# Optimization experiments

Measured on AMD Instinct MI355X. Metric: run time of the kernel, lower is better.

Reference implementation:

```python
import jax, jax.numpy as jnp
import numpy as np

K_SIZE = 7   # min_kernel_size (Parameter init value, clamped)
DIL = 2      # min_dilation (Parameter init value, clamped)


def conv2d(x, w, b):
    # x: (B, Cin, H, W), w: (Cout, Cin, kh, kw), stride 1, pad 1
    y = jax.lax.conv_general_dilated(
        x, w, window_strides=(1, 1), padding=((1, 1), (1, 1)),
        dimension_numbers=("NCHW", "OIHW", "NCHW"))
    return y + b[None, :, None, None]


def sincos_1d(length, dim, dtype):
    # standard sinusoidal encoding: (length, dim)
    half = dim // 2
    inv_freq = 1.0 / (10000.0 ** (jnp.arange(half, dtype=dtype) * 2.0 / dim))
    ang = jnp.arange(length, dtype=dtype)[:, None] * inv_freq[None, :]
    return jnp.concatenate([jnp.sin(ang), jnp.cos(ang)], axis=-1)


def positional_encoding_2d(H, W, C, dtype):
    # first C//2 channels encode height, last C//2 encode width -> (H, W, C)
    pe_h = sincos_1d(H, C // 2, dtype)  # (H, C/2)
    pe_w = sincos_1d(W, C // 2, dtype)  # (W, C/2)
    pe = jnp.concatenate([
        jnp.broadcast_to(pe_h[:, None, :], (H, W, C // 2)),
        jnp.broadcast_to(pe_w[None, :, :], (H, W, C // 2)),
    ], axis=-1)
    return pe


def na_indices(L, K, D):
    # NATTEN-style dilated neighborhood indices with border clamping.
    # Each position i attends within its dilation group g = i % D.
    i = jnp.arange(L)
    g = i % D
    r = i // D                       # rank within group
    Lg = (L - g + D - 1) // D        # group length
    start = jnp.clip(r - K // 2, 0, Lg - K)
    return g[:, None] + (start[:, None] + jnp.arange(K)[None, :]) * D  # (L, K)


def neighborhood_attention_2d(q, k, v, K, D):
    # q, k: (B, H, W, Cqk); v: (B, H, W, Cv); single head, scale = Cqk**-0.5
    B, H, W, Cqk = q.shape
    scale = jnp.asarray(Cqk, q.dtype) ** -0.5
    idx_h = na_indices(H, K, D)  # (H, K)
    idx_w = na_indices(W, K, D)  # (W, K)
    # gather neighborhood keys/values: (B, H, K, W, K, C)
    kn = k[:, idx_h][:, :, :, idx_w]
    vn = v[:, idx_h][:, :, :, idx_w]
    logits = jnp.einsum('bhwc,bhiwjc->bhwij', q * scale, kn)  # (B,H,W,K,K)
    p = jax.nn.softmax(logits.reshape(B, H, W, K * K), axis=-1)
    p = p.reshape(B, H, W, K, K)
    return jnp.einsum('bhwij,bhiwjc->bhwc', p, vn)


def setup_inputs() -> dict:
    key = jax.random.key(0)
    ks = jax.random.split(key, 4)
    B, Cin, H, W = 2, 64, 96, 96
    Ci, Co = 64, 128
    fan = Cin * 9
    s = (1.0 / fan) ** 0.5
    return {
        "x": jax.random.normal(ks[0], (B, Cin, H, W), dtype=jnp.float32),
        "wq": jax.random.normal(ks[1], (Ci, Cin, 3, 3), dtype=jnp.float32) * s,
        "bq": jnp.zeros((Ci,), dtype=jnp.float32),
        "wk": jax.random.normal(ks[2], (Ci, Cin, 3, 3), dtype=jnp.float32) * s,
        "bk": jnp.zeros((Ci,), dtype=jnp.float32),
        "wv": jax.random.normal(ks[3], (Co, Cin, 3, 3), dtype=jnp.float32) * s,
        "bv": jnp.zeros((Co,), dtype=jnp.float32),
    }


def reference(x, wq, bq, wk, bk, wv, bv):
    # Conv QKV (NCHW), then move to channels-last for attention
    q = jnp.transpose(conv2d(x, wq, bq), (0, 2, 3, 1))  # (B,H,W,Ci)
    k = jnp.transpose(conv2d(x, wk, bk), (0, 2, 3, 1))
    v = jnp.transpose(conv2d(x, wv, bv), (0, 2, 3, 1))  # (B,H,W,Co)
    B, H, W, Ci = q.shape
    pe = positional_encoding_2d(H, W, Ci, q.dtype)       # (H,W,Ci)
    pe_b = jnp.broadcast_to(pe[None], (B, H, W, Ci))
    q = jnp.concatenate([q, pe_b], axis=-1)              # (B,H,W,2*Ci)
    k = jnp.concatenate([k, pe_b], axis=-1)
    return neighborhood_attention_2d(q, k, v, K_SIZE, DIL)
```

## Files before the change

### kernel.cpp

```cpp
#include <hip/hip_runtime.h>
#include <math.h>

#define HWDIM 96
#define NPIX (HWDIM*HWDIM)
#define BATCH 2
#define CIN 64
#define CCAT 128

typedef __attribute__((ext_vector_type(8))) short bf16x8;
typedef __attribute__((ext_vector_type(4))) float f32x4;

__device__ __forceinline__ unsigned short f2bf(float f) {
    unsigned u = __builtin_bit_cast(unsigned, f);
    unsigned r = (u + 0x7FFFu + ((u >> 16) & 1u)) >> 16;
    return (unsigned short)r;
}

__global__ __launch_bounds__(256) void wb_kernel(
        const float* __restrict__ wq, const float* __restrict__ wk,
        const float* __restrict__ wv, unsigned short* __restrict__ wbT) {
    int base = blockIdx.x * 4096;
    int tid  = threadIdx.x;
    #pragma unroll
    for (int e = 0; e < 16; ++e) {
        int idx = base + e * 256 + tid;
        int t   = idx / (256 * 64);
        int rem = idx % (256 * 64);
        int co  = rem / 64;
        int ci  = rem % 64;
        float val;
        if (co < 64)        val = wq[(co * 64 + ci) * 9 + t];
        else if (co < 128)  val = wk[((co - 64) * 64 + ci) * 9 + t];
        else                val = wv[((co - 128) * 64 + ci) * 9 + t];
        wbT[(t * 256 + co) * 64 + ci] = f2bf(val);
    }
}

__global__ __launch_bounds__(256, 2) void conv_mfma(
        const float* __restrict__ x,
        const unsigned short* __restrict__ wbT,
        const float* __restrict__ bq, const float* __restrict__ bk,
        const float* __restrict__ bv,
        unsigned short* __restrict__ Qb, unsigned short* __restrict__ Kb,
        unsigned short* __restrict__ Vb) {
    __shared__ unsigned short xs[3 * 50 * 72];
    int bx      = blockIdx.x;
    int spatial = (bx & 7) * 48 + (bx >> 3);
    int b    = spatial / 192;
    int hh   = spatial % 192;
    int h    = hh >> 1;
    int w0   = (hh & 1) * 48;
    int co0  = blockIdx.y * 128;
    int tid  = threadIdx.x;

    #pragma unroll
    for (int g = 0; g < 5; ++g) {
        float vv[8];
        int   dst[8];
        bool  ok[8];
        #pragma unroll
        for (int e = 0; e < 8; ++e) {
            int i  = tid + (g * 8 + e) * 256;
            ok[e]  = (i < 9600);
            int ii = ok[e] ? i : 0;
            int r   = ii / 3200;
            int rem = ii % 3200;
            int ci  = rem / 50;
            int px  = rem % 50;
            int iy  = h - 1 + r;
            int ix  = w0 - 1 + px;
            float v = 0.f;
            if (ok[e] && iy >= 0 && iy < HWDIM && ix >= 0 && ix < HWDIM)
                v = x[((b * CIN + ci) * HWDIM + iy) * HWDIM + ix];
            vv[e]  = v;
            dst[e] = (r * 50 + px) * 72 + ci;
        }
        #pragma unroll
        for (int e = 0; e < 8; ++e)
            if (ok[e]) xs[dst[e]] = f2bf(vv[e]);
    }
    __syncthreads();

    int lane = tid & 63;
    int wv   = tid >> 6;
    int lw   = lane & 15;
    int ksub = (lane >> 4) * 8;
    int co_t = co0 + wv * 32;

    f32x4 acc[3][2];
    #pragma unroll
    for (int m = 0; m < 3; ++m)
        #pragma unroll
        for (int n = 0; n < 2; ++n) acc[m][n] = (f32x4){0.f, 0.f, 0.f, 0.f};

    #pragma unroll
    for (int half = 0; half < 2; ++half) {
        bf16x8 Bf[9][2];
        #pragma unroll
        for (int t = 0; t < 9; ++t) {
            const unsigned short* bp = wbT + ((t * 256 + co_t + lw) * 64) + half * 32 + ksub;
            Bf[t][0] = *(const bf16x8*)(bp);
            Bf[t][1] = *(const bf16x8*)(bp + 16 * 64);
        }
        #pragma unroll
        for (int t = 0; t < 9; ++t) {
            int kh = t / 3, kw = t % 3;
            const unsigned short* ap = xs + (kh * 50 + lw + kw) * 72 + half * 32 + ksub;
            bf16x8 A0 = *(const bf16x8*)(ap);
            bf16x8 A1 = *(const bf16x8*)(ap + 16 * 72);
            bf16x8 A2 = *(const bf16x8*)(ap + 32 * 72);
            acc[0][0] = __builtin_amdgcn_mfma_f32_16x16x32_bf16(A0, Bf[t][0], acc[0][0], 0, 0, 0);
            acc[0][1] = __builtin_amdgcn_mfma_f32_16x16x32_bf16(A0, Bf[t][1], acc[0][1], 0, 0, 0);
            acc[1][0] = __builtin_amdgcn_mfma_f32_16x16x32_bf16(A1, Bf[t][0], acc[1][0], 0, 0, 0);
            acc[1][1] = __builtin_amdgcn_mfma_f32_16x16x32_bf16(A1, Bf[t][1], acc[1][1], 0, 0, 0);
            acc[2][0] = __builtin_amdgcn_mfma_f32_16x16x32_bf16(A2, Bf[t][0], acc[2][0], 0, 0, 0);
            acc[2][1] = __builtin_amdgcn_mfma_f32_16x16x32_bf16(A2, Bf[t][1], acc[2][1], 0, 0, 0);
        }
    }

    __syncthreads();
    unsigned short* xs2 = xs;
    #pragma unroll
    for (int n = 0; n < 2; ++n) {
        int co_f = co_t + n * 16 + lw;
        float bval;
        if (co_f < 64)       bval = bq[co_f];
        else if (co_f < 128) bval = bk[co_f - 64];
        else                 bval = bv[co_f - 128];
        int chl = wv * 32 + n * 16 + lw;
        #pragma unroll
        for (int m = 0; m < 3; ++m) {
            int px = m * 16 + ((lane >> 4) << 2);
            #pragma unroll
            for (int r = 0; r < 4; ++r)
                xs2[(px + r) * 136 + chl] = f2bf(acc[m][n][r] + bval);
        }
    }
    __syncthreads();

    for (int i = tid; i < 768; i += 256) {
        int px  = i >> 4;
        int seg = i & 15;
        uint4 v = *(uint4*)&xs2[px * 136 + seg * 8];
        int pix = b * NPIX + h * HWDIM + w0 + px;
        int chl = seg * 8;
        if (co0 == 0) {
            if (chl < 64) *(uint4*)&Qb[pix * CCAT + chl]        = v;
            else          *(uint4*)&Kb[pix * CCAT + (chl - 64)] = v;
        } else {
            *(uint4*)&Vb[pix * CCAT + chl] = v;
        }
    }

    if (blockIdx.y == 0) {
        for (int i = tid; i < 48 * 64; i += 256) {
            int c  = i & 63;
            int pl = i >> 6;
            int w  = w0 + pl;
            int pos = (c < 32) ? h : w;
            int j   = c & 15;
            float f   = exp2f(-(float)j * 0.83048202372184059f);
            float ang = (float)pos * f;
            float val = ((c & 16) == 0) ? __sinf(ang) : __cosf(ang);
            unsigned short bvv = f2bf(val);
            int pix = b * NPIX + h * HWDIM + w;
            Qb[pix * CCAT + 64 + c] = bvv;
            Kb[pix * CCAT + 64 + c] = bvv;
        }
    }
}

#define KPAD 136
#define LGP  114

__global__ __launch_bounds__(256, 3) void natt_mfma(
        const unsigned short* __restrict__ Qb,
        const unsigned short* __restrict__ Kb,
        const unsigned short* __restrict__ Vb,
        float* __restrict__ out) {
    __shared__ unsigned short Vt[128 * KPAD];
    __shared__ unsigned short Pb[16 * KPAD];
    __shared__ float Lg[16 * LGP];

    int bid  = blockIdx.x;
    int xcd  = bid & 7;
    int slot = bid >> 3;
    int s3   = slot % 3;
    int rest = slot / 3;
    int code = xcd * 3 + s3;
    int b  = code / 12;
    int th = code % 12;
    int tw = rest % 12;
    int gg = rest / 12;
    int gh = gg & 1;
    int gw = gg >> 1;

    int rh0 = th * 4, rw0 = tw * 4;
    int base_h = min(max(rh0 - 3, 0), 41);
    int base_w = min(max(rw0 - 3, 0), 41);
    int tid = threadIdx.x;
    int lane = tid & 63;
    int wv   = tid >> 6;
    int lw   = lane & 15;
    int ks8  = (lane >> 4) * 8;

    uint4 va[4], vb2[4];
    int   vdst[4];
    #pragma unroll
    for (int j = 0; j < 4; ++j) {
        int c = tid + j * 256;
        bool valid = (j < 3) || (tid < 32);
        int pp = c >> 4, c8 = c & 15;
        int px0 = pp * 2, px1 = px0 + 1;
        int ih0 = px0 / 10, iw0 = px0 - ih0 * 10;
        int ih1 = px1 / 10, iw1 = px1 - ih1 * 10;
        int gp0 = b * NPIX + (gh + 2 * min(base_h + ih0, 47)) * HWDIM + (gw + 2 * min(base_w + iw0, 47));
        int gp1 = b * NPIX + (gh + 2 * min(base_h + ih1, 47)) * HWDIM + (gw + 2 * min(base_w + iw1, 47));
        if (valid) {
            va[j]  = *(const uint4*)(Vb + gp0 * CCAT + c8 * 8);
            vb2[j] = *(const uint4*)(Vb + gp1 * CCAT + c8 * 8);
        }
        vdst[j] = (c8 * 8) * KPAD + (px0 ^ ((c8 & 7) << 3));
    }

    for (int i = tid; i < 1024; i += 256) {
        int row = i >> 3, sg = i & 7;
        *(uint4*)(Vt + row * KPAD + 64 + sg * 8) = (uint4){0, 0, 0, 0};
    }

    const float scale = 0.08838834764831845f;
    {
        int qi = lw >> 2, qj = lw & 3;
        const unsigned short* qsrc = Qb +
            ((b * NPIX + (gh + 2 * (rh0 + qi)) * HWDIM + (gw + 2 * (rw0 + qj))) * CCAT) + ks8;
        bf16x8 A0 = *(const bf16x8*)(qsrc);
        bf16x8 A1 = *(const bf16x8*)(qsrc + 32);
        bf16x8 A2 = *(const bf16x8*)(qsrc + 64);
        bf16x8 A3 = *(const bf16x8*)(qsrc + 96);

        #pragma unroll
        for (int tt = 0; tt < 2; ++tt) {
            int tile = wv + tt * 4;
            if (tile < 7) {
                int px = min(tile * 16 + lw, 99);
                int ih = px / 10, iw = px - ih * 10;
                const unsigned short* ksrc = Kb +
                    ((b * NPIX + (gh + 2 * min(base_h + ih, 47)) * HWDIM
                               + (gw + 2 * min(base_w + iw, 47))) * CCAT) + ks8;
                bf16x8 B0 = *(const bf16x8*)(ksrc);
                bf16x8 B1 = *(const bf16x8*)(ksrc + 32);
                bf16x8 B2 = *(const bf16x8*)(ksrc + 64);
                bf16x8 B3 = *(const bf16x8*)(ksrc + 96);
                f32x4 acc = (f32x4){0.f, 0.f, 0.f, 0.f};
                __builtin_amdgcn_s_setprio(1);
                acc = __builtin_amdgcn_mfma_f32_16x16x32_bf16(A0, B0, acc, 0, 0, 0);
                acc = __builtin_amdgcn_mfma_f32_16x16x32_bf16(A1, B1, acc, 0, 0, 0);
                acc = __builtin_amdgcn_mfma_f32_16x16x32_bf16(A2, B2, acc, 0, 0, 0);
                acc = __builtin_amdgcn_mfma_f32_16x16x32_bf16(A3, B3, acc, 0, 0, 0);
                __builtin_amdgcn_s_setprio(0);
                #pragma unroll
                for (int r = 0; r < 4; ++r) {
                    int m = (lane >> 4) * 4 + r;
                    Lg[m * LGP + tile * 16 + lw] = acc[r] * scale;
                }
            }
        }
    }
    __syncthreads();

    #pragma unroll
    for (int j = 0; j < 4; ++j) {
        bool valid = (j < 3) || (tid < 32);
        if (valid) {
            unsigned short* vp = Vt + vdst[j];
            uint4 v0 = va[j], v1 = vb2[j];
            *(unsigned*)(vp + 0 * KPAD) = (v0.x & 0xFFFFu) | (v1.x << 16);
            *(unsigned*)(vp + 1 * KPAD) = (v0.x >> 16)     | (v1.x & 0xFFFF0000u);
            *(unsigned*)(vp + 2 * KPAD) = (v0.y & 0xFFFFu) | (v1.y << 16);
            *(unsigned*)(vp + 3 * KPAD) = (v0.y >> 16)     | (v1.y & 0xFFFF0000u);
            *(unsigned*)(vp + 4 * KPAD) = (v0.z & 0xFFFFu) | (v1.z << 16);
            *(unsigned*)(vp + 5 * KPAD) = (v0.z >> 16)     | (v1.z & 0xFFFF0000u);
            *(unsigned*)(vp + 6 * KPAD) = (v0.w & 0xFFFFu) | (v1.w << 16);
            *(unsigned*)(vp + 7 * KPAD) = (v0.w >> 16)     | (v1.w & 0xFFFF0000u);
        }
    }

    int q   = tid >> 4, k16 = tid & 15;
    {
        int qi  = q >> 2, qj = q & 3;
        int rh  = rh0 + qi, rw = rw0 + qj;
        int oh  = min(max(rh - 3, 0), 41) - base_h;
        int ow  = min(max(rw - 3, 0), 41) - base_w;

        float ev[4];
        int   en[4];
        float mx = -1e30f;
        #pragma unroll
        for (int u = 0; u < 4; ++u) {
            int idx = k16 + u * 16;
            if (idx < 49) {
                int i = idx / 7, j = idx - i * 7;
                int n = (oh + i) * 10 + ow + j;
                en[u] = n;
                float l = Lg[q * LGP + n];
                ev[u] = l;
                mx = fmaxf(mx, l);
            } else { en[u] = -1; ev[u] = 0.f; }
        }
        #pragma unroll
        for (int off = 8; off > 0; off >>= 1) mx = fmaxf(mx, __shfl_xor(mx, off));
        float s = 0.f;
        #pragma unroll
        for (int u = 0; u < 4; ++u)
            if (en[u] >= 0) { ev[u] = __expf(ev[u] - mx); s += ev[u]; }
        #pragma unroll
        for (int off = 8; off > 0; off >>= 1) s += __shfl_xor(s, off);
        float rs = 1.0f / s;
        *(uint4*)(Pb + q * KPAD + k16 * 8) = (uint4){0, 0, 0, 0};
        #pragma unroll
        for (int u = 0; u < 4; ++u)
            if (en[u] >= 0) Pb[q * KPAD + en[u]] = f2bf(ev[u] * rs);
    }
    __syncthreads();

    bf16x8 A4[4];
    #pragma unroll
    for (int kk = 0; kk < 4; ++kk)
        A4[kk] = *(const bf16x8*)(Pb + lw * KPAD + kk * 32 + ks8);

    __builtin_amdgcn_s_setprio(1);
    #pragma unroll
    for (int tt = 0; tt < 2; ++tt) {
        int tile = wv * 2 + tt;
        int row  = tile * 16 + lw;
        int sw   = ((row >> 3) & 7) << 3;
        const unsigned short* vrow = Vt + row * KPAD;
        f32x4 acc = (f32x4){0.f, 0.f, 0.f, 0.f};
        #pragma unroll
        for (int kk = 0; kk < 4; ++kk) {
            bf16x8 Bf = *(const bf16x8*)(vrow + ((kk * 32 + ks8) ^ sw));
            acc = __builtin_amdgcn_mfma_f32_16x16x32_bf16(A4[kk], Bf, acc, 0, 0, 0);
        }
        int ch = row;
        #pragma unroll
        for (int r = 0; r < 4; ++r) {
            int qq = (lane >> 4) * 4 + r;
            int qi = qq >> 2, qj = qq & 3;
            int gp = b * NPIX + (gh + 2 * (rh0 + qi)) * HWDIM + (gw + 2 * (rw0 + qj));
            out[gp * CCAT + ch] = acc[r];
        }
    }
    __builtin_amdgcn_s_setprio(0);
}

extern "C" void kernel_launch(void* const* d_in, const int* in_sizes, int n_in,
                              void* d_out, int out_size, void* d_ws, size_t ws_size,
                              hipStream_t stream) {
    const float* x  = (const float*)d_in[0];
    const float* wq = (const float*)d_in[1];
    const float* bq = (const float*)d_in[2];
    const float* wk = (const float*)d_in[3];
    const float* bk = (const float*)d_in[4];
    const float* wv = (const float*)d_in[5];
    const float* bv = (const float*)d_in[6];

    unsigned short* ws = (unsigned short*)d_ws;
    unsigned short* Qb  = ws;
    unsigned short* Kb  = Qb + BATCH * NPIX * CCAT;
    unsigned short* Vb  = Kb + BATCH * NPIX * CCAT;
    unsigned short* wbT = Vb + BATCH * NPIX * CCAT;

    hipLaunchKernelGGL(wb_kernel, dim3(36), dim3(256), 0, stream,
                       wq, wk, wv, wbT);
    hipLaunchKernelGGL(conv_mfma, dim3(384, 2), dim3(256), 0, stream,
                       x, wbT, bq, bk, bv, Qb, Kb, Vb);
    hipLaunchKernelGGL(natt_mfma, dim3(1152), dim3(256), 0, stream,
                       Qb, Kb, Vb, (float*)d_out);
}
```

Measured before the change: 45.26 us.

## Compute all 256 output channels per conv block and vectorize input staging

The conv kernel now has each block produce all 256 output channels (Q, K and V) for its 48-pixel strip, instead of splitting channels across two grid rows. This halves the grid, so the input tile is staged into shared memory once rather than twice. Input loads use float4 reads plus a small border pass instead of scalar loads. Weight fragments are loaded per tap inside the MFMA loop instead of being preloaded, the accumulator set doubles per wave, and occupancy is requested at 3 blocks per CU. The trade-off is fewer blocks, higher register pressure from the larger accumulator set, and a larger shared buffer for the epilogue.

```diff
diff --git a/kernel.cpp b/kernel.cpp
--- a/kernel.cpp
+++ b/kernel.cpp
@@ -36,48 +36,58 @@
     }
 }
 
-__global__ __launch_bounds__(256, 2) void conv_mfma(
+__global__ __launch_bounds__(256, 3) void conv_mfma(
         const float* __restrict__ x,
         const unsigned short* __restrict__ wbT,
         const float* __restrict__ bq, const float* __restrict__ bk,
         const float* __restrict__ bv,
         unsigned short* __restrict__ Qb, unsigned short* __restrict__ Kb,
         unsigned short* __restrict__ Vb) {
-    __shared__ unsigned short xs[3 * 50 * 72];
+    __shared__ unsigned short xs[12672];
     int bx      = blockIdx.x;
     int spatial = (bx & 7) * 48 + (bx >> 3);
     int b    = spatial / 192;
     int hh   = spatial % 192;
     int h    = hh >> 1;
     int w0   = (hh & 1) * 48;
-    int co0  = blockIdx.y * 128;
     int tid  = threadIdx.x;
 
     #pragma unroll
-    for (int g = 0; g < 5; ++g) {
-        float vv[8];
-        int   dst[8];
-        bool  ok[8];
-        #pragma unroll
-        for (int e = 0; e < 8; ++e) {
-            int i  = tid + (g * 8 + e) * 256;
-            ok[e]  = (i < 9600);
-            int ii = ok[e] ? i : 0;
-            int r   = ii / 3200;
-            int rem = ii % 3200;
-            int ci  = rem / 50;
-            int px  = rem % 50;
-            int iy  = h - 1 + r;
-            int ix  = w0 - 1 + px;
-            float v = 0.f;
-            if (ok[e] && iy >= 0 && iy < HWDIM && ix >= 0 && ix < HWDIM)
-                v = x[((b * CIN + ci) * HWDIM + iy) * HWDIM + ix];
-            vv[e]  = v;
-            dst[e] = (r * 50 + px) * 72 + ci;
-        }
-        #pragma unroll
-        for (int e = 0; e < 8; ++e)
-            if (ok[e]) xs[dst[e]] = f2bf(vv[e]);
+    for (int g = 0; g < 9; ++g) {
+        int i   = tid + g * 256;
+        int r   = i / 768;
+        int rem = i % 768;
+        int ci  = rem / 12;
+        int p4  = rem % 12;
+        int iy  = h - 1 + r;
+        float4 v = make_float4(0.f, 0.f, 0.f, 0.f);
+        if (iy >= 0 && iy < HWDIM)
+            v = *(const float4*)&x[((b * CIN + ci) * HWDIM + iy) * HWDIM + w0 + p4 * 4];
+        int base = (r * 50 + 1 + p4 * 4) * 72 + ci;
+        xs[base]       = f2bf(v.x);
+        xs[base + 72]  = f2bf(v.y);
+        xs[base + 144] = f2bf(v.z);
+        xs[base + 216] = f2bf(v.w);
+    }
+    {
+        int i = tid;
+        if (i < 192) {
+            #pragma unroll
+            for (int e = 0; e < 2; ++e) {
+                int ii   = i + e * 192;
+                int r    = ii / 128;
+                int rem  = ii % 128;
+                int ci   = rem >> 1;
+                int side = rem & 1;
+                int px   = side ? 49 : 0;
+                int ix   = w0 - 1 + px;
+                int iy   = h - 1 + r;
+                float v = 0.f;
+                if (iy >= 0 && iy < HWDIM && ix >= 0 && ix < HWDIM)
+                    v = x[((b * CIN + ci) * HWDIM + iy) * HWDIM + ix];
+                xs[(r * 50 + px) * 72 + ci] = f2bf(v);
+            }
+        }
     }
     __syncthreads();
 
@@ -85,23 +95,16 @@
     int wv   = tid >> 6;
     int lw   = lane & 15;
     int ksub = (lane >> 4) * 8;
-    int co_t = co0 + wv * 32;
-
-    f32x4 acc[3][2];
+    int co_t = wv * 64;
+
+    f32x4 acc[3][4];
     #pragma unroll
     for (int m = 0; m < 3; ++m)
         #pragma unroll
-        for (int n = 0; n < 2; ++n) acc[m][n] = (f32x4){0.f, 0.f, 0.f, 0.f};
+        for (int n = 0; n < 4; ++n) acc[m][n] = (f32x4){0.f, 0.f, 0.f, 0.f};
 
     #pragma unroll
     for (int half = 0; half < 2; ++half) {
-        bf16x8 Bf[9][2];
-        #pragma unroll
-        for (int t = 0; t < 9; ++t) {
-            const unsigned short* bp = wbT + ((t * 256 + co_t + lw) * 64) + half * 32 + ksub;
-            Bf[t][0] = *(const bf16x8*)(bp);
-            Bf[t][1] = *(const bf16x8*)(bp + 16 * 64);
-        }
         #pragma unroll
         for (int t = 0; t < 9; ++t) {
             int kh = t / 3, kw = t % 3;
@@ -109,64 +112,62 @@
             bf16x8 A0 = *(const bf16x8*)(ap);
             bf16x8 A1 = *(const bf16x8*)(ap + 16 * 72);
             bf16x8 A2 = *(const bf16x8*)(ap + 32 * 72);
-            acc[0][0] = __builtin_amdgcn_mfma_f32_16x16x32_bf16(A0, Bf[t][0], acc[0][0], 0, 0, 0);
-            acc[0][1] = __builtin_amdgcn_mfma_f32_16x16x32_bf16(A0, Bf[t][1], acc[0][1], 0, 0, 0);
-            acc[1][0] = __builtin_amdgcn_mfma_f32_16x16x32_bf16(A1, Bf[t][0], acc[1][0], 0, 0, 0);
-            acc[1][1] = __builtin_amdgcn_mfma_f32_16x16x32_bf16(A1, Bf[t][1], acc[1][1], 0, 0, 0);
-            acc[2][0] = __builtin_amdgcn_mfma_f32_16x16x32_bf16(A2, Bf[t][0], acc[2][0], 0, 0, 0);
-            acc[2][1] = __builtin_amdgcn_mfma_f32_16x16x32_bf16(A2, Bf[t][1], acc[2][1], 0, 0, 0);
+            const unsigned short* bp = wbT + ((t * 256 + co_t + lw) * 64) + half * 32 + ksub;
+            #pragma unroll
+            for (int n = 0; n < 4; ++n) {
+                bf16x8 Bf = *(const bf16x8*)(bp + n * (16 * 64));
+                acc[0][n] = __builtin_amdgcn_mfma_f32_16x16x32_bf16(A0, Bf, acc[0][n], 0, 0, 0);
+                acc[1][n] = __builtin_amdgcn_mfma_f32_16x16x32_bf16(A1, Bf, acc[1][n], 0, 0, 0);
+                acc[2][n] = __builtin_amdgcn_mfma_f32_16x16x32_bf16(A2, Bf, acc[2][n], 0, 0, 0);
+            }
         }
     }
 
     __syncthreads();
     unsigned short* xs2 = xs;
     #pragma unroll
-    for (int n = 0; n < 2; ++n) {
+    for (int n = 0; n < 4; ++n) {
         int co_f = co_t + n * 16 + lw;
         float bval;
         if (co_f < 64)       bval = bq[co_f];
         else if (co_f < 128) bval = bk[co_f - 64];
         else                 bval = bv[co_f - 128];
-        int chl = wv * 32 + n * 16 + lw;
         #pragma unroll
         for (int m = 0; m < 3; ++m) {
             int px = m * 16 + ((lane >> 4) << 2);
             #pragma unroll
             for (int r = 0; r < 4; ++r)
-                xs2[(px + r) * 136 + chl] = f2bf(acc[m][n][r] + bval);
-        }
-    }
-    __syncthreads();
-
-    for (int i = tid; i < 768; i += 256) {
-        int px  = i >> 4;
-        int seg = i & 15;
-        uint4 v = *(uint4*)&xs2[px * 136 + seg * 8];
+                xs2[(px + r) * 264 + co_f] = f2bf(acc[m][n][r] + bval);
+        }
+    }
+    __syncthreads();
+
+    #pragma unroll
+    for (int e = 0; e < 6; ++e) {
+        int i   = tid + e * 256;
+        int px  = i >> 5;
+        int seg = i & 31;
+        uint4 v = *(uint4*)&xs2[px * 264 + seg * 8];
         int pix = b * NPIX + h * HWDIM + w0 + px;
         int chl = seg * 8;
-        if (co0 == 0) {
-            if (chl < 64) *(uint4*)&Qb[pix * CCAT + chl]        = v;
-            else          *(uint4*)&Kb[pix * CCAT + (chl - 64)] = v;
-        } else {
-            *(uint4*)&Vb[pix * CCAT + chl] = v;
-        }
-    }
-
-    if (blockIdx.y == 0) {
-        for (int i = tid; i < 48 * 64; i += 256) {
-            int c  = i & 63;
-            int pl = i >> 6;
-            int w  = w0 + pl;
-            int pos = (c < 32) ? h : w;
-            int j   = c & 15;
-            float f   = exp2f(-(float)j * 0.83048202372184059f);
-            float ang = (float)pos * f;
-            float val = ((c & 16) == 0) ? __sinf(ang) : __cosf(ang);
-            unsigned short bvv = f2bf(val);
-            int pix = b * NPIX + h * HWDIM + w;
-            Qb[pix * CCAT + 64 + c] = bvv;
-            Kb[pix * CCAT + 64 + c] = bvv;
-        }
+        if (chl < 64)        *(uint4*)&Qb[pix * CCAT + chl]         = v;
+        else if (chl < 128)  *(uint4*)&Kb[pix * CCAT + (chl - 64)]  = v;
+        else                 *(uint4*)&Vb[pix * CCAT + (chl - 128)] = v;
+    }
+
+    for (int i = tid; i < 48 * 64; i += 256) {
+        int c  = i & 63;
+        int pl = i >> 6;
+        int w  = w0 + pl;
+        int pos = (c < 32) ? h : w;
+        int j   = c & 15;
+        float f   = exp2f(-(float)j * 0.83048202372184059f);
+        float ang = (float)pos * f;
+        float val = ((c & 16) == 0) ? __sinf(ang) : __cosf(ang);
+        unsigned short bvv = f2bf(val);
+        int pix = b * NPIX + h * HWDIM + w;
+        Qb[pix * CCAT + 64 + c] = bvv;
+        Kb[pix * CCAT + 64 + c] = bvv;
     }
 }
 
@@ -372,7 +373,7 @@
 
     hipLaunchKernelGGL(wb_kernel, dim3(36), dim3(256), 0, stream,
                        wq, wk, wv, wbT);
-    hipLaunchKernelGGL(conv_mfma, dim3(384, 2), dim3(256), 0, stream,
+    hipLaunchKernelGGL(conv_mfma, dim3(384), dim3(256), 0, stream,
                        x, wbT, bq, bk, bv, Qb, Kb, Vb);
     hipLaunchKernelGGL(natt_mfma, dim3(1152), dim3(256), 0, stream,
                        Qb, Kb, Vb, (float*)d_out);
```

After: 50.96 us. 12.6% more time.
